# Performance work log

Hardware: AMD Instinct MI355X
Metric: run time of the kernel (lower is better)

The kernel has to match this reference:

```python
import jax, jax.numpy as jnp
import numpy as np

B, S, D, T = 512, 65536, 256, 10   # graphs, substructures, emb_dim, num_tasks
THRESHOLD = 0.4                    # CausalGNN threshold default
MEMBER_P = 0.002                   # ~131 substructures per graph


def setup_inputs() -> dict:
    key = jax.random.key(0)
    ks = jax.random.split(key, 8)
    def w(k, shape):
        fan_in = shape[0]
        return jax.random.normal(k, shape, jnp.float32) / np.float32(np.sqrt(fan_in))
    return {
        "h_graph": jax.random.normal(ks[0], (B, D), jnp.float32),
        "h_sub":   jax.random.normal(ks[1], (S, D), jnp.float32),
        "W1": w(ks[2], (D, 2 * D)),  "b1": jnp.zeros((2 * D,), jnp.float32),
        "W2": w(ks[3], (2 * D, 1)),  "b2": jnp.zeros((1,), jnp.float32),
        "Wc": w(ks[4], (2 * D, T)),  "bc": jnp.zeros((T,), jnp.float32),
        # dense [B,S] bool membership: mask[i,j] = substructure j belongs to graph i
        "mask": jax.random.bernoulli(ks[5], MEMBER_P, (B, S)),
    }


def _l2_normalize(x, eps=1e-12):  # F.normalize(p=2, dim=1)
    n = jnp.linalg.norm(x, axis=1, keepdims=True)
    return x / jnp.maximum(n, eps)


def reference(h_graph, h_sub, W1, b1, W2, b2, Wc, bc, mask):
    # SubMaskGenerator: Linear -> ReLU -> Dropout(eval=identity) -> Linear -> sigmoid, squeeze
    gate_logits = (jax.nn.relu(h_sub @ W1 + b1) @ W2 + b2)[:, 0]      # [S]
    subgraph_mask = jax.nn.sigmoid(gate_logits)                        # [S]

    # fused masked segment mean (replaces per-graph python loop + host sync):
    # valid[i,j] = (sub j in graph i) & (gate > threshold)
    valid = mask & (subgraph_mask > THRESHOLD)                         # [B,S] bool
    w = valid.astype(h_sub.dtype)
    counts = w.sum(axis=1, keepdims=True)                              # [B,1]
    sums = w @ h_sub                                                   # [B,D]
    h_sub_aligned = jnp.where(counts > 0, sums / jnp.maximum(counts, 1.0), 0.0)

    h_sub_norm = _l2_normalize(h_sub_aligned)
    h_graph_norm = _l2_normalize(h_graph)
    # F.cosine_similarity(dim=1, eps=1e-8) on the already-normalized vectors
    na = jnp.linalg.norm(h_sub_norm, axis=1)
    ng = jnp.linalg.norm(h_graph_norm, axis=1)
    cos = (h_sub_norm * h_graph_norm).sum(axis=1) / (
        jnp.maximum(na, 1e-8) * jnp.maximum(ng, 1e-8))
    cosine_loss = 1.0 - cos.mean()

    h_combined = jnp.concatenate([h_graph, h_sub_aligned], axis=1)     # [B,2D]
    logits = h_combined @ Wc + bc                                      # [B,T]
    return logits, cosine_loss, subgraph_mask
```

## Files before the change

### kernel.cpp

```cpp
#include <hip/hip_runtime.h>
#include <math.h>

#define D 256
#define H 512
#define TT 10
#define THRESH 0.4f
#define KS 8
#define NSPLIT 16

typedef __attribute__((ext_vector_type(8))) _Float16 half8;
typedef __attribute__((ext_vector_type(4))) float f32x4;

__global__ __launch_bounds__(256) void w1_prep(const float* __restrict__ W1,
                                               short* __restrict__ W1s)
{
    const int tid = blockIdx.x * 256 + threadIdx.x;
    const int lane = tid & 63;
    const int cell = tid >> 6;
    const int k = cell & 7;
    const int n = cell >> 3;
    const int row0 = k * 32 + (lane >> 4) * 8;
    const int col = n * 16 + (lane & 15);
    _Float16 h8[8];
    #pragma unroll
    for (int i = 0; i < 8; ++i)
        h8[i] = (_Float16)W1[(size_t)(row0 + i) * H + col];
    *reinterpret_cast<half8*>(W1s + (((size_t)n * 8 + k) * 64 + lane) * 8) =
        *reinterpret_cast<half8*>(h8);
}

__global__ __launch_bounds__(256, 1) void gate_mfma(
    const float* __restrict__ h_sub,
    const short* __restrict__ W1s,
    const float* __restrict__ b1,
    const float* __restrict__ W2,
    const float* __restrict__ b2,
    float* __restrict__ submask,
    unsigned* __restrict__ gbits)
{
    __shared__ __align__(16) short sB[65536];
    __shared__ float sb1[H], sw2[H];
    const int tid = threadIdx.x;
    const int lane = tid & 63;
    const int w = tid >> 6;
    const int base = blockIdx.x * 256 + w * 64;
    const float bb = b2[0];

    auto stagePhase = [&](int p) {
        const char* gp = (const char*)W1s + (size_t)p * 131072 + (size_t)tid * 16;
        char* lp0 = (char*)sB + (size_t)tid * 16;
        #pragma unroll
        for (int i = 0; i < 32; ++i) {
            __builtin_amdgcn_global_load_lds(
                (const __attribute__((address_space(1))) void*)(gp + i * 4096),
                (__attribute__((address_space(3))) void*)(lp0 + i * 4096),
                16, 0, 0);
        }
    };

    stagePhase(0);
    sb1[tid] = b1[tid];       sb1[tid + 256] = b1[tid + 256];
    sw2[tid] = W2[tid];       sw2[tid + 256] = W2[tid + 256];

    half8 af[4][KS];
    #pragma unroll
    for (int s = 0; s < 4; ++s) {
        const int row = base + s * 16 + (lane & 15);
        const float* rp = h_sub + (size_t)row * D + (lane >> 4) * 8;
        #pragma unroll
        for (int k = 0; k < KS; ++k) {
            float x[8];
            *reinterpret_cast<float4*>(&x[0]) =
                *reinterpret_cast<const float4*>(rp + k * 32);
            *reinterpret_cast<float4*>(&x[4]) =
                *reinterpret_cast<const float4*>(rp + k * 32 + 4);
            _Float16 h8[8];
            #pragma unroll
            for (int i = 0; i < 8; ++i) h8[i] = (_Float16)x[i];
            af[s][k] = *reinterpret_cast<half8*>(h8);
        }
    }

    float lp[4][4];
    #pragma unroll
    for (int s = 0; s < 4; ++s)
        #pragma unroll
        for (int j = 0; j < 4; ++j) lp[s][j] = 0.f;

    #pragma unroll
    for (int p = 0; p < 2; ++p) {
        __syncthreads();

        #pragma unroll
        for (int nn = 0; nn < 16; ++nn) {
            const int n = (nn + w * 4) & 15;
            f32x4 acc[4];
            #pragma unroll
            for (int s = 0; s < 4; ++s) acc[s] = (f32x4){0.f,0.f,0.f,0.f};

            __builtin_amdgcn_s_setprio(1);
            #pragma unroll
            for (int k = 0; k < KS; ++k) {
                half8 bh = *reinterpret_cast<const half8*>(
                    sB + ((n * 8 + k) * 64 + lane) * 8);
                acc[0] = __builtin_amdgcn_mfma_f32_16x16x32_f16(af[0][k], bh, acc[0], 0, 0, 0);
                acc[1] = __builtin_amdgcn_mfma_f32_16x16x32_f16(af[1][k], bh, acc[1], 0, 0, 0);
                acc[2] = __builtin_amdgcn_mfma_f32_16x16x32_f16(af[2][k], bh, acc[2], 0, 0, 0);
                acc[3] = __builtin_amdgcn_mfma_f32_16x16x32_f16(af[3][k], bh, acc[3], 0, 0, 0);
            }
            __builtin_amdgcn_s_setprio(0);

            const int hc = p * 256 + n * 16 + (lane & 15);
            const float b1h = sb1[hc], w2h = sw2[hc];
            #pragma unroll
            for (int s = 0; s < 4; ++s)
                #pragma unroll
                for (int j = 0; j < 4; ++j) {
                    float v = acc[s][j] + b1h;
                    v = v > 0.f ? v : 0.f;
                    lp[s][j] = fmaf(v, w2h, lp[s][j]);
                }
        }

        if (p == 0) {
            __syncthreads();
            stagePhase(1);
        }
    }

    #pragma unroll
    for (int m = 1; m < 16; m <<= 1)
        #pragma unroll
        for (int s = 0; s < 4; ++s)
            #pragma unroll
            for (int j = 0; j < 4; ++j)
                lp[s][j] += __shfl_xor(lp[s][j], m);

    const int g = lane >> 4;
    unsigned b0 = 0, b1w = 0;
    float sig[4][4];
    #pragma unroll
    for (int s = 0; s < 4; ++s)
        #pragma unroll
        for (int j = 0; j < 4; ++j) {
            sig[s][j] = 1.f / (1.f + expf(-(lp[s][j] + bb)));
            const int r = s * 16 + g * 4 + j;
            if (sig[s][j] > THRESH) {
                if (r < 32) b0 |= 1u << r;
                else        b1w |= 1u << (r - 32);
            }
        }
    b0  |= __shfl_xor(b0, 16);  b0  |= __shfl_xor(b0, 32);
    b1w |= __shfl_xor(b1w, 16); b1w |= __shfl_xor(b1w, 32);
    if (lane == 0) {
        gbits[blockIdx.x * 8 + w * 2 + 0] = b0;
        gbits[blockIdx.x * 8 + w * 2 + 1] = b1w;
    }
    if ((lane & 15) == 0)
        #pragma unroll
        for (int s = 0; s < 4; ++s)
            #pragma unroll
            for (int j = 0; j < 4; ++j)
                submask[base + s * 16 + g * 4 + j] = sig[s][j];
}

__global__ __launch_bounds__(256) void seg_scan(
    const float* __restrict__ h_sub,
    const int*   __restrict__ mask,
    const unsigned* __restrict__ gbits,
    float* __restrict__ psum,
    int*   __restrict__ pcnt,
    int S)
{
    const int i = blockIdx.x / NSPLIT;
    const int p = blockIdx.x % NSPLIT;
    const int tid = threadIdx.x;
    const int lane = tid & 63;
    const int w = tid >> 6;
    const int seg = S / NSPLIT;
    const int start = p * seg;
    const int* mrow = mask + (size_t)i * S + start;

    __shared__ unsigned sbits[4096 / 32];
    if (tid < seg / 32) sbits[tid] = gbits[(start >> 5) + tid];

    const int wbase = w * 1024;
    int4 m4[4];
    #pragma unroll
    for (int it = 0; it < 4; ++it)
        m4[it] = *reinterpret_cast<const int4*>(mrow + wbase + it * 256 + (lane << 2));

    __syncthreads();

    float4 acc = make_float4(0.f, 0.f, 0.f, 0.f);
    int cnt = 0;

    #pragma unroll
    for (int it = 0; it < 4; ++it) {
        const int j0 = wbase + it * 256 + (lane << 2);
        const unsigned bw = sbits[j0 >> 5];
        const int sh = j0 & 31;
        unsigned long long bal[4];
        bal[0] = __ballot((m4[it].x != 0) & ((bw >> (sh + 0)) & 1u));
        bal[1] = __ballot((m4[it].y != 0) & ((bw >> (sh + 1)) & 1u));
        bal[2] = __ballot((m4[it].z != 0) & ((bw >> (sh + 2)) & 1u));
        bal[3] = __ballot((m4[it].w != 0) & ((bw >> (sh + 3)) & 1u));
        #pragma unroll
        for (int s = 0; s < 4; ++s) {
            unsigned long long b = bal[s];
            while (b) {
                int t = __builtin_ctzll(b);
                b &= b - 1;
                int jj = start + wbase + it * 256 + (t << 2) + s;
                float4 hv = *reinterpret_cast<const float4*>(
                    h_sub + (size_t)jj * D + (lane << 2));
                acc.x += hv.x; acc.y += hv.y; acc.z += hv.z; acc.w += hv.w;
                cnt++;
            }
        }
    }

    __shared__ float ssum[4][D];
    __shared__ int   scnt[4];
    *reinterpret_cast<float4*>(&ssum[w][lane << 2]) = acc;
    if (lane == 0) scnt[w] = cnt;
    __syncthreads();

    float a = ssum[0][tid] + ssum[1][tid] + ssum[2][tid] + ssum[3][tid];
    psum[(size_t)blockIdx.x * D + tid] = a;
    if (tid == 0) pcnt[blockIdx.x] = scnt[0] + scnt[1] + scnt[2] + scnt[3];
}

__global__ __launch_bounds__(256) void seg_combine(
    const float* __restrict__ h_graph,
    const float* __restrict__ psum,
    const int*   __restrict__ pcnt,
    const float* __restrict__ Wc,
    const float* __restrict__ bc,
    float* __restrict__ logits,
    float* __restrict__ cos_ws)
{
    const int i = blockIdx.x;
    const int tid = threadIdx.x;
    const int lane = tid & 63;
    const int w = tid >> 6;

    float a = 0.f;
    int c = 0;
    #pragma unroll
    for (int p = 0; p < NSPLIT; ++p) {
        a += psum[((size_t)i * NSPLIT + p) * D + tid];
        c += pcnt[i * NSPLIT + p];
    }
    a = (c > 0) ? (a / (float)c) : 0.f;
    const float g = h_graph[(size_t)i * D + tid];

    float r0 = a * a, r1 = g * g, r2 = a * g;
    #pragma unroll
    for (int m = 1; m < 64; m <<= 1) {
        r0 += __shfl_xor(r0, m);
        r1 += __shfl_xor(r1, m);
        r2 += __shfl_xor(r2, m);
    }
    __shared__ float red[4][3];
    if (lane == 0) { red[w][0] = r0; red[w][1] = r1; red[w][2] = r2; }
    __syncthreads();
    if (tid == 0) {
        float a2 = red[0][0] + red[1][0] + red[2][0] + red[3][0];
        float g2 = red[0][1] + red[1][1] + red[2][1] + red[3][1];
        float ag = red[0][2] + red[1][2] + red[2][2] + red[3][2];
        float an = sqrtf(a2), gn = sqrtf(g2);
        float cs = (c > 0) ? (ag / (fmaxf(an, 1e-12f) * fmaxf(gn, 1e-12f))) : 0.f;
        cos_ws[i] = cs;
    }

    float lg[TT];
    #pragma unroll
    for (int t = 0; t < TT; ++t)
        lg[t] = g * Wc[(size_t)tid * TT + t] + a * Wc[(size_t)(D + tid) * TT + t];
    #pragma unroll
    for (int m = 1; m < 64; m <<= 1)
        #pragma unroll
        for (int t = 0; t < TT; ++t) lg[t] += __shfl_xor(lg[t], m);
    __shared__ float lpart[4][TT];
    if (lane == 0)
        #pragma unroll
        for (int t = 0; t < TT; ++t) lpart[w][t] = lg[t];
    __syncthreads();
    if (tid < TT)
        logits[(size_t)i * TT + tid] =
            lpart[0][tid] + lpart[1][tid] + lpart[2][tid] + lpart[3][tid] + bc[tid];
}

__global__ void loss_kernel(const float* __restrict__ cos_ws,
                            float* __restrict__ out, int B)
{
    const int lane = threadIdx.x;
    float s = 0.f;
    for (int i = lane; i < B; i += 64) s += cos_ws[i];
    #pragma unroll
    for (int m = 1; m < 64; m <<= 1) s += __shfl_xor(s, m);
    if (lane == 0) out[0] = 1.0f - s / (float)B;
}

extern "C" void kernel_launch(void* const* d_in, const int* in_sizes, int n_in,
                              void* d_out, int out_size, void* d_ws, size_t ws_size,
                              hipStream_t stream)
{
    const float* h_graph = (const float*)d_in[0];
    const float* h_sub   = (const float*)d_in[1];
    const float* W1      = (const float*)d_in[2];
    const float* b1      = (const float*)d_in[3];
    const float* W2      = (const float*)d_in[4];
    const float* b2      = (const float*)d_in[5];
    const float* Wc      = (const float*)d_in[6];
    const float* bc      = (const float*)d_in[7];
    const int*   mask    = (const int*)d_in[8];

    const int B = in_sizes[0] / D;
    const int S = in_sizes[1] / D;

    float* out     = (float*)d_out;
    float* logits  = out;
    float* loss    = out + (size_t)B * TT;
    float* submask = loss + 1;

    char* ws = (char*)d_ws;
    short*    W1s    = (short*)ws;
    unsigned* gbits  = (unsigned*)(ws + 512 * 1024);
    int*      pcnt   = (int*)(ws + 528 * 1024);
    float*    cos_ws = (float*)(ws + 576 * 1024);
    float*    psum   = (float*)(ws + 1024 * 1024);

    w1_prep<<<64, 256, 0, stream>>>(W1, W1s);
    gate_mfma<<<S / 256, 256, 0, stream>>>(h_sub, W1s, b1, W2, b2, submask, gbits);
    seg_scan<<<B * NSPLIT, 256, 0, stream>>>(h_sub, mask, gbits, psum, pcnt, S);
    seg_combine<<<B, 256, 0, stream>>>(h_graph, psum, pcnt, Wc, bc, logits, cos_ws);
    loss_kernel<<<1, 64, 0, stream>>>(cos_ws, loss, B);
}
```

Measured before the change: 77.37 us.

## Overlap mask bit-compaction with gate MFMA using extra warps in fused kernel

The gate kernel grows to 512 threads. The four new waves read the dense int membership mask and compact it into ballot bitmasks while the original four waves run the MFMA gate computation, with work interleaved across block barriers. seg_scan then reads the compact bitmask instead of the 128MB int mask, so the mask read moves off the dependent path and overlaps with compute-bound MFMA work. The cost is a larger gate block, extra barriers that tie the two roles together, and a new workspace buffer.

New measurement: 93.72 us. 1.21x slower.

```diff
diff --git a/kernel.cpp b/kernel.cpp
--- a/kernel.cpp
+++ b/kernel.cpp
@@ -29,20 +29,23 @@
         *reinterpret_cast<half8*>(h8);
 }
 
-__global__ __launch_bounds__(256, 1) void gate_mfma(
+__global__ __launch_bounds__(512, 1) void gate_fused(
     const float* __restrict__ h_sub,
     const short* __restrict__ W1s,
     const float* __restrict__ b1,
     const float* __restrict__ W2,
     const float* __restrict__ b2,
+    const int*   __restrict__ mask,
     float* __restrict__ submask,
-    unsigned* __restrict__ gbits)
+    unsigned* __restrict__ gbits,
+    unsigned long long* __restrict__ cmask)
 {
     __shared__ __align__(16) short sB[65536];
     __shared__ float sb1[H], sw2[H];
     const int tid = threadIdx.x;
     const int lane = tid & 63;
     const int w = tid >> 6;
+    const bool isGate = (w < 4);
     const int base = blockIdx.x * 256 + w * 64;
     const float bb = b2[0];
 
@@ -58,46 +61,70 @@
         }
     };
 
-    stagePhase(0);
-    sb1[tid] = b1[tid];       sb1[tid + 256] = b1[tid + 256];
-    sw2[tid] = W2[tid];       sw2[tid + 256] = W2[tid + 256];
+    const int mw = blockIdx.x * 4 + (w - 4);
+    const size_t g0 = (size_t)mw * 128;
+    auto maskChunk = [&](int lo, int hi) {
+        for (int g = lo; g < hi; g += 4) {
+            int4 m4[4];
+            #pragma unroll
+            for (int u = 0; u < 4; ++u)
+                m4[u] = *reinterpret_cast<const int4*>(
+                    mask + (g0 + g + u) * 256 + (lane << 2));
+            #pragma unroll
+            for (int u = 0; u < 4; ++u) {
+                unsigned long long c0 = __ballot(m4[u].x != 0);
+                unsigned long long c1 = __ballot(m4[u].y != 0);
+                unsigned long long c2 = __ballot(m4[u].z != 0);
+                unsigned long long c3 = __ballot(m4[u].w != 0);
+                if (lane == 0) {
+                    unsigned long long* cp = cmask + (g0 + g + u) * 4;
+                    cp[0] = c0; cp[1] = c1; cp[2] = c2; cp[3] = c3;
+                }
+            }
+        }
+    };
 
     half8 af[4][KS];
-    #pragma unroll
-    for (int s = 0; s < 4; ++s) {
-        const int row = base + s * 16 + (lane & 15);
-        const float* rp = h_sub + (size_t)row * D + (lane >> 4) * 8;
-        #pragma unroll
-        for (int k = 0; k < KS; ++k) {
-            float x[8];
-            *reinterpret_cast<float4*>(&x[0]) =
-                *reinterpret_cast<const float4*>(rp + k * 32);
-            *reinterpret_cast<float4*>(&x[4]) =
-                *reinterpret_cast<const float4*>(rp + k * 32 + 4);
-            _Float16 h8[8];
-            #pragma unroll
-            for (int i = 0; i < 8; ++i) h8[i] = (_Float16)x[i];
-            af[s][k] = *reinterpret_cast<half8*>(h8);
-        }
-    }
-
     float lp[4][4];
-    #pragma unroll
-    for (int s = 0; s < 4; ++s)
-        #pragma unroll
-        for (int j = 0; j < 4; ++j) lp[s][j] = 0.f;
-
-    #pragma unroll
-    for (int p = 0; p < 2; ++p) {
-        __syncthreads();
-
+
+    if (isGate) {
+        stagePhase(0);
+        sb1[tid] = b1[tid];       sb1[tid + 256] = b1[tid + 256];
+        sw2[tid] = W2[tid];       sw2[tid + 256] = W2[tid + 256];
+        #pragma unroll
+        for (int s = 0; s < 4; ++s) {
+            const int row = base + s * 16 + (lane & 15);
+            const float* rp = h_sub + (size_t)row * D + (lane >> 4) * 8;
+            #pragma unroll
+            for (int k = 0; k < KS; ++k) {
+                float x[8];
+                *reinterpret_cast<float4*>(&x[0]) =
+                    *reinterpret_cast<const float4*>(rp + k * 32);
+                *reinterpret_cast<float4*>(&x[4]) =
+                    *reinterpret_cast<const float4*>(rp + k * 32 + 4);
+                _Float16 h8[8];
+                #pragma unroll
+                for (int i = 0; i < 8; ++i) h8[i] = (_Float16)x[i];
+                af[s][k] = *reinterpret_cast<half8*>(h8);
+            }
+        }
+        #pragma unroll
+        for (int s = 0; s < 4; ++s)
+            #pragma unroll
+            for (int j = 0; j < 4; ++j) lp[s][j] = 0.f;
+    } else {
+        maskChunk(0, 32);
+    }
+
+    __syncthreads();
+
+    if (isGate) {
         #pragma unroll
         for (int nn = 0; nn < 16; ++nn) {
             const int n = (nn + w * 4) & 15;
             f32x4 acc[4];
             #pragma unroll
             for (int s = 0; s < 4; ++s) acc[s] = (f32x4){0.f,0.f,0.f,0.f};
-
             __builtin_amdgcn_s_setprio(1);
             #pragma unroll
             for (int k = 0; k < KS; ++k) {
@@ -109,8 +136,7 @@
                 acc[3] = __builtin_amdgcn_mfma_f32_16x16x32_f16(af[3][k], bh, acc[3], 0, 0, 0);
             }
             __builtin_amdgcn_s_setprio(0);
-
-            const int hc = p * 256 + n * 16 + (lane & 15);
+            const int hc = n * 16 + (lane & 15);
             const float b1h = sb1[hc], w2h = sw2[hc];
             #pragma unroll
             for (int s = 0; s < 4; ++s)
@@ -121,52 +147,89 @@
                     lp[s][j] = fmaf(v, w2h, lp[s][j]);
                 }
         }
-
-        if (p == 0) {
-            __syncthreads();
-            stagePhase(1);
-        }
-    }
-
-    #pragma unroll
-    for (int m = 1; m < 16; m <<= 1)
+    } else {
+        maskChunk(32, 80);
+    }
+
+    __syncthreads();
+
+    if (isGate) stagePhase(1);
+    else        maskChunk(80, 88);
+
+    __syncthreads();
+
+    if (isGate) {
+        #pragma unroll
+        for (int nn = 0; nn < 16; ++nn) {
+            const int n = (nn + w * 4) & 15;
+            f32x4 acc[4];
+            #pragma unroll
+            for (int s = 0; s < 4; ++s) acc[s] = (f32x4){0.f,0.f,0.f,0.f};
+            __builtin_amdgcn_s_setprio(1);
+            #pragma unroll
+            for (int k = 0; k < KS; ++k) {
+                half8 bh = *reinterpret_cast<const half8*>(
+                    sB + ((n * 8 + k) * 64 + lane) * 8);
+                acc[0] = __builtin_amdgcn_mfma_f32_16x16x32_f16(af[0][k], bh, acc[0], 0, 0, 0);
+                acc[1] = __builtin_amdgcn_mfma_f32_16x16x32_f16(af[1][k], bh, acc[1], 0, 0, 0);
+                acc[2] = __builtin_amdgcn_mfma_f32_16x16x32_f16(af[2][k], bh, acc[2], 0, 0, 0);
+                acc[3] = __builtin_amdgcn_mfma_f32_16x16x32_f16(af[3][k], bh, acc[3], 0, 0, 0);
+            }
+            __builtin_amdgcn_s_setprio(0);
+            const int hc = 256 + n * 16 + (lane & 15);
+            const float b1h = sb1[hc], w2h = sw2[hc];
+            #pragma unroll
+            for (int s = 0; s < 4; ++s)
+                #pragma unroll
+                for (int j = 0; j < 4; ++j) {
+                    float v = acc[s][j] + b1h;
+                    v = v > 0.f ? v : 0.f;
+                    lp[s][j] = fmaf(v, w2h, lp[s][j]);
+                }
+        }
+
+        #pragma unroll
+        for (int m = 1; m < 16; m <<= 1)
+            #pragma unroll
+            for (int s = 0; s < 4; ++s)
+                #pragma unroll
+                for (int j = 0; j < 4; ++j)
+                    lp[s][j] += __shfl_xor(lp[s][j], m);
+
+        const int g = lane >> 4;
+        unsigned b0 = 0, b1w = 0;
+        float sig[4][4];
         #pragma unroll
         for (int s = 0; s < 4; ++s)
             #pragma unroll
-            for (int j = 0; j < 4; ++j)
-                lp[s][j] += __shfl_xor(lp[s][j], m);
-
-    const int g = lane >> 4;
-    unsigned b0 = 0, b1w = 0;
-    float sig[4][4];
-    #pragma unroll
-    for (int s = 0; s < 4; ++s)
-        #pragma unroll
-        for (int j = 0; j < 4; ++j) {
-            sig[s][j] = 1.f / (1.f + expf(-(lp[s][j] + bb)));
-            const int r = s * 16 + g * 4 + j;
-            if (sig[s][j] > THRESH) {
-                if (r < 32) b0 |= 1u << r;
-                else        b1w |= 1u << (r - 32);
-            }
-        }
-    b0  |= __shfl_xor(b0, 16);  b0  |= __shfl_xor(b0, 32);
-    b1w |= __shfl_xor(b1w, 16); b1w |= __shfl_xor(b1w, 32);
-    if (lane == 0) {
-        gbits[blockIdx.x * 8 + w * 2 + 0] = b0;
-        gbits[blockIdx.x * 8 + w * 2 + 1] = b1w;
-    }
-    if ((lane & 15) == 0)
-        #pragma unroll
-        for (int s = 0; s < 4; ++s)
-            #pragma unroll
-            for (int j = 0; j < 4; ++j)
-                submask[base + s * 16 + g * 4 + j] = sig[s][j];
+            for (int j = 0; j < 4; ++j) {
+                sig[s][j] = 1.f / (1.f + expf(-(lp[s][j] + bb)));
+                const int r = s * 16 + g * 4 + j;
+                if (sig[s][j] > THRESH) {
+                    if (r < 32) b0 |= 1u << r;
+                    else        b1w |= 1u << (r - 32);
+                }
+            }
+        b0  |= __shfl_xor(b0, 16);  b0  |= __shfl_xor(b0, 32);
+        b1w |= __shfl_xor(b1w, 16); b1w |= __shfl_xor(b1w, 32);
+        if (lane == 0) {
+            gbits[blockIdx.x * 8 + w * 2 + 0] = b0;
+            gbits[blockIdx.x * 8 + w * 2 + 1] = b1w;
+        }
+        if ((lane & 15) == 0)
+            #pragma unroll
+            for (int s = 0; s < 4; ++s)
+                #pragma unroll
+                for (int j = 0; j < 4; ++j)
+                    submask[base + s * 16 + g * 4 + j] = sig[s][j];
+    } else {
+        maskChunk(88, 128);
+    }
 }
 
 __global__ __launch_bounds__(256) void seg_scan(
     const float* __restrict__ h_sub,
-    const int*   __restrict__ mask,
+    const unsigned long long* __restrict__ cmask,
     const unsigned* __restrict__ gbits,
     float* __restrict__ psum,
     int*   __restrict__ pcnt,
@@ -179,17 +242,11 @@
     const int w = tid >> 6;
     const int seg = S / NSPLIT;
     const int start = p * seg;
-    const int* mrow = mask + (size_t)i * S + start;
+    const unsigned long long* cm =
+        cmask + ((size_t)i * (S / 256) + (size_t)p * (seg / 256)) * 4;
 
     __shared__ unsigned sbits[4096 / 32];
     if (tid < seg / 32) sbits[tid] = gbits[(start >> 5) + tid];
-
-    const int wbase = w * 1024;
-    int4 m4[4];
-    #pragma unroll
-    for (int it = 0; it < 4; ++it)
-        m4[it] = *reinterpret_cast<const int4*>(mrow + wbase + it * 256 + (lane << 2));
-
     __syncthreads();
 
     float4 acc = make_float4(0.f, 0.f, 0.f, 0.f);
@@ -197,21 +254,22 @@
 
     #pragma unroll
     for (int it = 0; it < 4; ++it) {
-        const int j0 = wbase + it * 256 + (lane << 2);
+        const int g = w * 4 + it;
+        const int j0 = g * 256 + (lane << 2);
         const unsigned bw = sbits[j0 >> 5];
         const int sh = j0 & 31;
         unsigned long long bal[4];
-        bal[0] = __ballot((m4[it].x != 0) & ((bw >> (sh + 0)) & 1u));
-        bal[1] = __ballot((m4[it].y != 0) & ((bw >> (sh + 1)) & 1u));
-        bal[2] = __ballot((m4[it].z != 0) & ((bw >> (sh + 2)) & 1u));
-        bal[3] = __ballot((m4[it].w != 0) & ((bw >> (sh + 3)) & 1u));
+        bal[0] = __ballot((bw >> (sh + 0)) & 1u) & cm[(size_t)g * 4 + 0];
+        bal[1] = __ballot((bw >> (sh + 1)) & 1u) & cm[(size_t)g * 4 + 1];
+        bal[2] = __ballot((bw >> (sh + 2)) & 1u) & cm[(size_t)g * 4 + 2];
+        bal[3] = __ballot((bw >> (sh + 3)) & 1u) & cm[(size_t)g * 4 + 3];
         #pragma unroll
         for (int s = 0; s < 4; ++s) {
             unsigned long long b = bal[s];
             while (b) {
                 int t = __builtin_ctzll(b);
                 b &= b - 1;
-                int jj = start + wbase + it * 256 + (t << 2) + s;
+                int jj = start + g * 256 + (t << 2) + s;
                 float4 hv = *reinterpret_cast<const float4*>(
                     h_sub + (size_t)jj * D + (lane << 2));
                 acc.x += hv.x; acc.y += hv.y; acc.z += hv.z; acc.w += hv.w;
@@ -331,10 +389,13 @@
     int*      pcnt   = (int*)(ws + 528 * 1024);
     float*    cos_ws = (float*)(ws + 576 * 1024);
     float*    psum   = (float*)(ws + 1024 * 1024);
+    unsigned long long* cmask =
+        (unsigned long long*)(ws + 16 * 1024 * 1024);
 
     w1_prep<<<64, 256, 0, stream>>>(W1, W1s);
-    gate_mfma<<<S / 256, 256, 0, stream>>>(h_sub, W1s, b1, W2, b2, submask, gbits);
-    seg_scan<<<B * NSPLIT, 256, 0, stream>>>(h_sub, mask, gbits, psum, pcnt, S);
+    gate_fused<<<S / 256, 512, 0, stream>>>(
+        h_sub, W1s, b1, W2, b2, mask, submask, gbits, cmask);
+    seg_scan<<<B * NSPLIT, 256, 0, stream>>>(h_sub, cmask, gbits, psum, pcnt, S);
     seg_combine<<<B, 256, 0, stream>>>(h_graph, psum, pcnt, Wc, bc, logits, cos_ws);
     loss_kernel<<<1, 64, 0, stream>>>(cos_ws, loss, B);
 }
```
